# Kernel optimization log

Hardware: AMD Instinct MI355X
Metric: run time of the kernel (lower is better)

## Reference

```python
import jax, jax.numpy as jnp
import numpy as np

B, N = 65536, 8
OBS0, OBS1, OBS2 = 6, 1024, 7
H, HC, NA = 64, 128, 2


def _glorot(key, shape):
    fan_in = shape[0]
    lim = 1.0 / np.sqrt(fan_in)
    return jax.random.uniform(key, shape, jnp.float32, -lim, lim)


def setup_inputs() -> dict:
    key = jax.random.key(0)
    ks = jax.random.split(key, 24)
    state0 = jax.random.normal(ks[0], (B, OBS0), jnp.float32)
    state1 = jax.random.normal(ks[1], (B, OBS1), jnp.float32)
    state2 = jax.random.normal(ks[2], (B, N, OBS2), jnp.float32)
    keep = (jax.random.uniform(ks[3], (B, N, 1)) > 0.35) | (jnp.arange(N)[None, :, None] == 0)
    state2 = state2 * keep.astype(jnp.float32)
    return {
        "state0": state0, "state1": state1, "state2": state2,
        "W0": _glorot(ks[4], (OBS0, H)), "b0": jnp.zeros((H,), jnp.float32),
        "Wg": _glorot(ks[5], (OBS1, H)), "bg": jnp.zeros((H,), jnp.float32),
        "Ws1": _glorot(ks[6], (OBS2, H)), "bs1": jnp.zeros((H,), jnp.float32),
        "Ws2": _glorot(ks[7], (H, H)), "bs2": jnp.zeros((H,), jnp.float32),
        "Wq": _glorot(ks[8], (H, H)),
        "Wk": _glorot(ks[9], (H, H)),
        "Wv": _glorot(ks[10], (H, H)),
        "Wc1": _glorot(ks[11], (3 * H, HC)), "bc1": jnp.zeros((HC,), jnp.float32),
        "Wc2": _glorot(ks[12], (HC, HC)), "bc2": jnp.zeros((HC,), jnp.float32),
        "Wc3": _glorot(ks[13], (HC, NA)), "bc3": jnp.zeros((NA,), jnp.float32),
    }


def reference(state0, state1, state2,
              W0, b0, Wg, bg, Ws1, bs1, Ws2, bs2,
              Wq, Wk, Wv, Wc1, bc1, Wc2, bc2, Wc3, bc3):
    own_e = jax.nn.relu(state0 @ W0 + b0)                      # [B, 64]
    env_e = jax.nn.relu(state1 @ Wg + bg)                      # [B, 64]
    intru_e = jax.nn.relu(state2 @ Ws1 + bs1)                  # [B, N, 64]
    intru_e = jax.nn.relu(intru_e @ Ws2 + bs2)                 # [B, N, 64]

    q = own_e @ Wq                                             # [B, 64]
    k = intru_e @ Wk                                           # [B, N, 64]
    v = intru_e @ Wv                                           # [B, N, 64]

    # mask: True where the neighbor slot is non-padding (mean over feats != 0)
    mask = jnp.mean(state2, axis=2, keepdims=True) != 0        # [B, N, 1] bool

    score = jnp.einsum('bnd,bd->bn', k, q)[..., None]          # [B, N, 1]
    score_m = jnp.where(mask, score, -jnp.inf)
    alpha = jax.nn.softmax(score_m / np.sqrt(H), axis=1)       # [B, N, 1]
    alpha_m = jnp.where(mask, alpha, 0.0)
    v_att = jnp.sum(v * alpha_m, axis=1)                       # [B, 64]

    concat = jnp.concatenate((own_e, env_e, v_att), axis=1)    # [B, 192]
    h = jax.nn.relu(concat @ Wc1 + bc1)
    h = jax.nn.relu(h @ Wc2 + bc2)
    return jnp.tanh(h @ Wc3 + bc3)                             # [B, n_actions]
```

## Files before the change

### kernel.cpp

```cpp
#include <hip/hip_runtime.h>
#include <math.h>


typedef float f32x4 __attribute__((ext_vector_type(4)));
typedef float f32x4u __attribute__((ext_vector_type(4), aligned(4)));
typedef float f32x2u __attribute__((ext_vector_type(2), aligned(4)));
typedef __bf16 bf16x8 __attribute__((ext_vector_type(8)));
typedef unsigned short u16x8 __attribute__((ext_vector_type(8)));

#define DI __device__ __forceinline__

DI unsigned short f2bf_u(float f) {
  unsigned u = __builtin_bit_cast(unsigned, f);
  u += 0x7fffu + ((u >> 16) & 1u);
  return (unsigned short)(u >> 16);
}
DI float bfu2f(unsigned short s) {
  unsigned u = ((unsigned)s) << 16;
  return __builtin_bit_cast(float, u);
}
DI u16x8 cvt8(f32x4 x, f32x4 y) {
  bf16x8 r;
  r[0] = (__bf16)x[0]; r[1] = (__bf16)x[1]; r[2] = (__bf16)x[2]; r[3] = (__bf16)x[3];
  r[4] = (__bf16)y[0]; r[5] = (__bf16)y[1]; r[6] = (__bf16)y[2]; r[7] = (__bf16)y[3];
  return __builtin_bit_cast(u16x8, r);
}
DI f32x4 mfma16(u16x8 a, u16x8 b, f32x4 c) {
  return __builtin_amdgcn_mfma_f32_16x16x32_bf16(
      __builtin_bit_cast(bf16x8, a), __builtin_bit_cast(bf16x8, b), c, 0, 0, 0);
}
DI void gload_lds16(const void* g, void* l) {
  typedef __attribute__((address_space(1))) const unsigned GU;
  typedef __attribute__((address_space(3))) unsigned LU;
  __builtin_amdgcn_global_load_lds((GU*)g, (LU*)l, 16, 0, 0);
}


constexpr size_t WS_WGF = 0;
constexpr size_t WS_WS2 = 131072;
constexpr size_t WS_WV  = 139264;
constexpr size_t WS_MQK = 147456;
constexpr size_t WS_WC1 = 155648;
constexpr size_t WS_WC2 = 204800;

__global__ __launch_bounds__(256) void k_prep(
    const float* __restrict__ Wg, const float* __restrict__ Ws2,
    const float* __restrict__ Wv, const float* __restrict__ Wq,
    const float* __restrict__ Wk, const float* __restrict__ Wc1,
    const float* __restrict__ Wc2,
    unsigned short* __restrict__ wgf, unsigned short* __restrict__ ws2f,
    unsigned short* __restrict__ wvf, unsigned short* __restrict__ mqkf,
    unsigned short* __restrict__ wc1f, unsigned short* __restrict__ wc2f) {
  const int idx = blockIdx.x * 256 + threadIdx.x;
  const float* src = nullptr;
  unsigned short* dst;
  int i, ntm, NC;
  bool is_mqk = false;
  if (idx < 65536)      { src = Wg;  dst = wgf;  i = idx;          ntm = 2; NC = 64;  }
  else if (idx < 69632) { src = Ws2; dst = ws2f; i = idx - 65536;  ntm = 2; NC = 64;  }
  else if (idx < 73728) { src = Wv;  dst = wvf;  i = idx - 69632;  ntm = 2; NC = 64;  }
  else if (idx < 77824) { is_mqk = true; dst = mqkf; i = idx - 73728; ntm = 2; NC = 64; }
  else if (idx < 102400){ src = Wc1; dst = wc1f; i = idx - 77824;  ntm = 3; NC = 128; }
  else                  { src = Wc2; dst = wc2f; i = idx - 102400; ntm = 3; NC = 128; }
  const int j = i & 7, ln = (i >> 3) & 63, t2 = i >> 9;
  const int nt = t2 & ((1 << ntm) - 1), kt = t2 >> ntm;
  const int k = kt * 32 + (ln >> 4) * 8 + j, n = nt * 16 + (ln & 15);
  float val;
  if (is_mqk) {
    const f32x4* qp = (const f32x4*)(Wq + k * 64);
    const f32x4* kp = (const f32x4*)(Wk + n * 64);
    float acc = 0.f;
#pragma unroll
    for (int d4 = 0; d4 < 16; ++d4) {
      const f32x4 a = qp[d4], b = kp[d4];
#pragma unroll
      for (int e = 0; e < 4; ++e) acc = fmaf(a[e], b[e], acc);
    }
    val = acc;
  } else {
    val = src[k * NC + n];
  }
  dst[i] = f2bf_u(val);
}

__global__ __launch_bounds__(256, 3) void k_main(
    const float* __restrict__ s0, const float* __restrict__ s1,
    const float* __restrict__ s2,
    const float* __restrict__ W0, const float* __restrict__ b0v,
    const unsigned short* __restrict__ wgf, const float* __restrict__ bg,
    const float* __restrict__ Ws1, const float* __restrict__ bs1,
    const unsigned short* __restrict__ ws2f, const float* __restrict__ bs2,
    const unsigned short* __restrict__ wvf, const unsigned short* __restrict__ mqkf,
    const unsigned short* __restrict__ wc1f, const float* __restrict__ bc1,
    const unsigned short* __restrict__ wc2f, const float* __restrict__ bc2,
    const float* __restrict__ Wc3, const float* __restrict__ bc3,
    float* __restrict__ out) {
  __shared__ __align__(16) char smem[54272];
  u16x8* EF = (u16x8*)smem;
  unsigned short* EFs = (unsigned short*)smem;
  u16x8* H1F = (u16x8*)smem;
  unsigned short* H1Fs = (unsigned short*)smem;
  float* H2 = (float*)(smem + 8192);
  u16x8* CF = (u16x8*)(smem + 32768);
  unsigned short* CFs = (unsigned short*)(smem + 32768);
  float* QK = (float*)(smem + 45056);
  u16x8* SEF = (u16x8*)(smem + 45056);
  float* SC = (float*)(smem + 53248);

  const int tid = threadIdx.x;
  const int lane = tid & 63, wave = tid >> 6;
  const int lo = lane & 15, q = lane >> 4;
  const int bbase = blockIdx.x * 32;

  const int bl8 = tid >> 3, n8 = tid & 7;
  const float* s2p = s2 + ((size_t)(bbase + bl8) * 8 + n8) * 7;
  const f32x4u x03 = *(const f32x4u*)s2p;
  const f32x2u x45 = *(const f32x2u*)(s2p + 4);
  const float x6 = s2p[6];
  const float* s0p = s0 + (size_t)(bbase + bl8) * 6;
  const f32x4u y03 = *(const f32x4u*)s0p;
  const f32x2u y45 = *(const f32x2u*)(s0p + 4);

  {
    const int mt = wave & 1, ntb = wave >> 1;
    const char* s1b = (const char*)(s1 + (size_t)bbase * 1024);

    int srow[4], scol[4];
#pragma unroll
    for (int i = 0; i < 4; ++i) {
      const int T = (i * 256 + tid) * 16;
      srow[i] = T >> 9;
      scol[i] = (T & 511) ^ ((srow[i] & 7) << 4);
    }
    auto stage = [&](char* dst, int c) {
      const int srcb = c * 512;
#pragma unroll
      for (int i = 0; i < 4; ++i)
        gload_lds16(s1b + (size_t)srow[i] * 4096 + srcb + scol[i],
                    dst + (i * 256 + tid) * 16);
    };

    f32x4 acc0 = {}, acc1 = {};
    const int row = mt * 16 + lo;
    const int sw = (row & 7) << 4;
    const u16x8* wgfp = (const u16x8*)wgf + (ntb * 2) * 64 + lane;

    auto compute = [&](const char* src, int c) {
#pragma unroll
      for (int kt = 0; kt < 4; ++kt) {
        const int base = row * 512 + kt * 128 + q * 32;
        const f32x4 alo = *(const f32x4*)(src + (base ^ sw));
        const f32x4 ahi = *(const f32x4*)(src + ((base + 16) ^ sw));
        const int ktg = c * 4 + kt;
        const u16x8 b0 = wgfp[(ktg * 4 + 0) * 64];
        const u16x8 b1 = wgfp[(ktg * 4 + 1) * 64];
        const u16x8 af = cvt8(alo, ahi);
        acc0 = mfma16(af, b0, acc0);
        acc1 = mfma16(af, b1, acc1);
      }
    };

    stage(smem, 0);
    __syncthreads();
#pragma unroll
    for (int cc = 0; cc < 4; ++cc) {
      stage(smem + 16384, cc * 2 + 1);
      compute(smem, cc * 2);
      __syncthreads();
      if (cc < 3) stage(smem, cc * 2 + 2);
      compute(smem + 16384, cc * 2 + 1);
      __syncthreads();
    }

#pragma unroll
    for (int ni = 0; ni < 2; ++ni) {
      const f32x4 a = ni ? acc1 : acc0;
      const int h = (ntb * 2 + ni) * 16 + lo;
      const float bias = bg[h];
#pragma unroll
      for (int ri = 0; ri < 4; ++ri) {
        const float v = fmaxf(a[ri] + bias, 0.f);
        CFs[((mt * 6 + 2 + (h >> 5)) * 64 +
             ((((h >> 3) & 3) << 4) | (q * 4 + ri))) * 8 + (h & 7)] = f2bf_u(v);
      }
    }
  }

  bool maskreg;
  {
    float xv[7] = {x03[0], x03[1], x03[2], x03[3], x45[0], x45[1], x6};
    const float sum = xv[0] + xv[1] + xv[2] + xv[3] + xv[4] + xv[5] + xv[6];
    maskreg = (sum != 0.f);
    const int mt = tid >> 4, rl = tid & 15;
#pragma unroll
    for (int c = 0; c < 8; ++c) {
      float a[8];
#pragma unroll
      for (int i = 0; i < 8; ++i) a[i] = bs1[c * 8 + i];
#pragma unroll
      for (int j = 0; j < 7; ++j) {
        const float* wr = Ws1 + j * 64 + c * 8;
#pragma unroll
        for (int i = 0; i < 8; ++i) a[i] = fmaf(xv[j], wr[i], a[i]);
      }
      u16x8 pk;
#pragma unroll
      for (int i = 0; i < 8; ++i) pk[i] = f2bf_u(fmaxf(a[i], 0.f));
      EF[(mt * 2 + (c >> 2)) * 64 + (((c & 3) << 4) | rl)] = pk;
    }
  }
  __syncthreads();

  {
    u16x8 Bf[4][2];
#pragma unroll
    for (int nt = 0; nt < 4; ++nt)
#pragma unroll
      for (int kt = 0; kt < 2; ++kt)
        Bf[nt][kt] = ((const u16x8*)ws2f)[(kt * 4 + nt) * 64 + lane];
    float bias[4];
#pragma unroll
    for (int nt = 0; nt < 4; ++nt) bias[nt] = bs2[nt * 16 + lo];
#pragma unroll
    for (int mi = 0; mi < 4; ++mi) {
      const int mt = wave * 4 + mi;
      const u16x8 A0 = EF[(mt * 2 + 0) * 64 + lane];
      const u16x8 A1 = EF[(mt * 2 + 1) * 64 + lane];
      f32x4 acc[4] = {};
#pragma unroll
      for (int nt = 0; nt < 4; ++nt) {
        acc[nt] = mfma16(A0, Bf[nt][0], acc[nt]);
        acc[nt] = mfma16(A1, Bf[nt][1], acc[nt]);
      }
#pragma unroll
      for (int nt = 0; nt < 4; ++nt) {
        const int h = nt * 16 + lo;
#pragma unroll
        for (int ri = 0; ri < 4; ++ri) {
          const float v = fmaxf(acc[nt][ri] + bias[nt], 0.f);
          const int rr = mt * 16 + q * 4 + ri;
          EFs[((mt * 2 + (h >> 5)) * 64 + ((((h >> 3) & 3) << 4) | (rr & 15))) * 8 +
              (h & 7)] = f2bf_u(v);
        }
      }
    }
  }
  __syncthreads();

  {
    const int mt = bl8 >> 4, fl = ((n8 & 3) << 4) | (bl8 & 15), kt = n8 >> 2;
    const float yv[6] = {y03[0], y03[1], y03[2], y03[3], y45[0], y45[1]};
    float a[8];
#pragma unroll
    for (int i = 0; i < 8; ++i) a[i] = b0v[n8 * 8 + i];
#pragma unroll
    for (int j = 0; j < 6; ++j) {
      const float* wr = W0 + j * 64 + n8 * 8;
#pragma unroll
      for (int i = 0; i < 8; ++i) a[i] = fmaf(yv[j], wr[i], a[i]);
    }
    u16x8 pk;
#pragma unroll
    for (int i = 0; i < 8; ++i) pk[i] = f2bf_u(fmaxf(a[i], 0.f));
    CF[(mt * 6 + kt) * 64 + fl] = pk;
  }
  __syncthreads();

  {
#pragma unroll
    for (int pp = 0; pp < 2; ++pp) {
      const int pr = wave * 2 + pp, mt = pr >> 2, nt = pr & 3;
      const u16x8 A0 = CF[(mt * 6 + 0) * 64 + lane];
      const u16x8 A1 = CF[(mt * 6 + 1) * 64 + lane];
      const u16x8 B0 = ((const u16x8*)mqkf)[(0 * 4 + nt) * 64 + lane];
      const u16x8 B1 = ((const u16x8*)mqkf)[(1 * 4 + nt) * 64 + lane];
      f32x4 acc = {};
      acc = mfma16(A0, B0, acc);
      acc = mfma16(A1, B1, acc);
#pragma unroll
      for (int ri = 0; ri < 4; ++ri)
        QK[(mt * 16 + q * 4 + ri) * 64 + nt * 16 + lo] = acc[ri];
    }
  }
  __syncthreads();

  {
    const int r = tid, bl = r >> 3, mt = r >> 4, rl = r & 15;
    float dot = 0.f;
#pragma unroll
    for (int c = 0; c < 8; ++c) {
      const u16x8 e = EF[(mt * 2 + (c >> 2)) * 64 + (((c & 3) << 4) | rl)];
      const float* qkp = QK + bl * 64 + c * 8;
      const f32x4 qa = *(const f32x4*)(qkp);
      const f32x4 qb = *(const f32x4*)(qkp + 4);
#pragma unroll
      for (int i = 0; i < 4; ++i) dot = fmaf(bfu2f(e[i]), qa[i], dot);
#pragma unroll
      for (int i = 0; i < 4; ++i) dot = fmaf(bfu2f(e[4 + i]), qb[i], dot);
    }
    SC[r] = maskreg ? dot * 0.125f : -1e30f;
  }
  __syncthreads();

  if (tid < 32) {
    float s[8];
#pragma unroll
    for (int n = 0; n < 8; ++n) s[n] = SC[tid * 8 + n];
    float mx = s[0];
#pragma unroll
    for (int n = 1; n < 8; ++n) mx = fmaxf(mx, s[n]);
    float e[8], sum = 0.f;
#pragma unroll
    for (int n = 0; n < 8; ++n) { e[n] = __expf(s[n] - mx); sum += e[n]; }
    const float inv = 1.f / sum;
#pragma unroll
    for (int n = 0; n < 8; ++n) SC[tid * 8 + n] = e[n] * inv;
  }
  __syncthreads();

  {
    float al[8];
#pragma unroll
    for (int n = 0; n < 8; ++n) al[n] = SC[bl8 * 8 + n];
    float a[8] = {0.f, 0.f, 0.f, 0.f, 0.f, 0.f, 0.f, 0.f};
#pragma unroll
    for (int n = 0; n < 8; ++n) {
      const int rr = bl8 * 8 + n;
      const u16x8 e =
          EF[((rr >> 4) * 2 + (n8 >> 2)) * 64 + (((n8 & 3) << 4) | (rr & 15))];
#pragma unroll
      for (int i = 0; i < 8; ++i) a[i] = fmaf(al[n], bfu2f(e[i]), a[i]);
    }
    u16x8 pk;
#pragma unroll
    for (int i = 0; i < 8; ++i) pk[i] = f2bf_u(a[i]);
    SEF[((bl8 >> 4) * 2 + (n8 >> 2)) * 64 + (((n8 & 3) << 4) | (bl8 & 15))] = pk;
  }
  __syncthreads();

  {
#pragma unroll
    for (int pp = 0; pp < 2; ++pp) {
      const int pr = wave * 2 + pp, mt = pr >> 2, nt = pr & 3;
      const u16x8 A0 = SEF[(mt * 2 + 0) * 64 + lane];
      const u16x8 A1 = SEF[(mt * 2 + 1) * 64 + lane];
      const u16x8 B0 = ((const u16x8*)wvf)[(0 * 4 + nt) * 64 + lane];
      const u16x8 B1 = ((const u16x8*)wvf)[(1 * 4 + nt) * 64 + lane];
      f32x4 acc = {};
      acc = mfma16(A0, B0, acc);
      acc = mfma16(A1, B1, acc);
      const int h = nt * 16 + lo;
#pragma unroll
      for (int ri = 0; ri < 4; ++ri) {
        const int rr = mt * 16 + q * 4 + ri;
        CFs[((mt * 6 + 4 + (h >> 5)) * 64 + ((((h >> 3) & 3) << 4) | (rr & 15))) * 8 +
            (h & 7)] = f2bf_u(acc[ri]);
      }
    }
  }
  __syncthreads();

  {
    const int mt = wave & 1, ntb = (wave >> 1) * 4;
    u16x8 A[6];
#pragma unroll
    for (int kt = 0; kt < 6; ++kt) A[kt] = CF[(mt * 6 + kt) * 64 + lane];
#pragma unroll
    for (int ni = 0; ni < 4; ++ni) {
      const int nt = ntb + ni;
      f32x4 acc = {};
#pragma unroll
      for (int kt = 0; kt < 6; ++kt) {
        const u16x8 Bf = ((const u16x8*)wc1f)[(kt * 8 + nt) * 64 + lane];
        acc = mfma16(A[kt], Bf, acc);
      }
      const float bias = bc1[nt * 16 + lo];
      const int h = nt * 16 + lo;
#pragma unroll
      for (int ri = 0; ri < 4; ++ri) {
        const float v = fmaxf(acc[ri] + bias, 0.f);
        const int rr = mt * 16 + q * 4 + ri;
        H1Fs[((mt * 4 + (h >> 5)) * 64 + ((((h >> 3) & 3) << 4) | (rr & 15))) * 8 +
             (h & 7)] = f2bf_u(v);
      }
    }
  }
  __syncthreads();

  {
    const int mt = wave & 1, ntb = (wave >> 1) * 4;
    u16x8 A[4];
#pragma unroll
    for (int kt = 0; kt < 4; ++kt) A[kt] = H1F[(mt * 4 + kt) * 64 + lane];
#pragma unroll
    for (int ni = 0; ni < 4; ++ni) {
      const int nt = ntb + ni;
      f32x4 acc = {};
#pragma unroll
      for (int kt = 0; kt < 4; ++kt) {
        const u16x8 Bf = ((const u16x8*)wc2f)[(kt * 8 + nt) * 64 + lane];
        acc = mfma16(A[kt], Bf, acc);
      }
      const float bias = bc2[nt * 16 + lo];
#pragma unroll
      for (int ri = 0; ri < 4; ++ri)
        H2[(mt * 16 + q * 4 + ri) * 132 + nt * 16 + lo] =
            fmaxf(acc[ri] + bias, 0.f);
    }
  }
  __syncthreads();

  {
    const int kq = n8 >> 1, a = n8 & 1;
    const f32x4* h4 = (const f32x4*)(H2 + bl8 * 132 + kq * 32);
    const float* wr = Wc3 + kq * 64;
    float acc = 0.f;
#pragma unroll
    for (int j4 = 0; j4 < 8; ++j4) {
      const f32x4 hv = h4[j4];
#pragma unroll
      for (int e = 0; e < 4; ++e) acc = fmaf(hv[e], wr[(j4 * 4 + e) * 2 + a], acc);
    }
    acc += __shfl_down(acc, 2);
    acc += __shfl_down(acc, 4);
    if (kq == 0) out[(size_t)(bbase + bl8) * 2 + a] = tanhf(acc + bc3[a]);
  }
}

extern "C" void kernel_launch(void* const* d_in, const int* in_sizes, int n_in,
                              void* d_out, int out_size, void* d_ws, size_t ws_size,
                              hipStream_t stream) {
  const float* s0  = (const float*)d_in[0];
  const float* s1  = (const float*)d_in[1];
  const float* s2  = (const float*)d_in[2];
  const float* W0  = (const float*)d_in[3];
  const float* b0  = (const float*)d_in[4];
  const float* Wg  = (const float*)d_in[5];
  const float* bg  = (const float*)d_in[6];
  const float* Ws1 = (const float*)d_in[7];
  const float* bs1 = (const float*)d_in[8];
  const float* Ws2 = (const float*)d_in[9];
  const float* bs2 = (const float*)d_in[10];
  const float* Wq  = (const float*)d_in[11];
  const float* Wk  = (const float*)d_in[12];
  const float* Wv  = (const float*)d_in[13];
  const float* Wc1 = (const float*)d_in[14];
  const float* bc1 = (const float*)d_in[15];
  const float* Wc2 = (const float*)d_in[16];
  const float* bc2 = (const float*)d_in[17];
  const float* Wc3 = (const float*)d_in[18];
  const float* bc3 = (const float*)d_in[19];

  char* ws = (char*)d_ws;
  unsigned short* wgf  = (unsigned short*)(ws + WS_WGF);
  unsigned short* ws2f = (unsigned short*)(ws + WS_WS2);
  unsigned short* wvf  = (unsigned short*)(ws + WS_WV);
  unsigned short* mqkf = (unsigned short*)(ws + WS_MQK);
  unsigned short* wc1f = (unsigned short*)(ws + WS_WC1);
  unsigned short* wc2f = (unsigned short*)(ws + WS_WC2);

  hipLaunchKernelGGL(k_prep, dim3(464), dim3(256), 0, stream, Wg, Ws2, Wv, Wq,
                     Wk, Wc1, Wc2, wgf, ws2f, wvf, mqkf, wc1f, wc2f);
  hipLaunchKernelGGL(k_main, dim3(2048), dim3(256), 0, stream, s0, s1, s2, W0,
                     b0, wgf, bg, Ws1, bs1, ws2f, bs2, wvf, mqkf, wc1f, bc1,
                     wc2f, bc2, Wc3, bc3, (float*)d_out);
}
```

Before: 453.4 us.

## Restructure per-wave staging and wave-local attention to cut block barriers

The state1 GEMM now stages a private 8KB LDS buffer per wave, with k split across wave pairs and reduced through LDS, replacing the block-wide double-buffered pipeline and its many __syncthreads. Each wave now owns a 16-row M tile through the attention stages. own_e stays in registers and feeds both the q projection and the Wc1 GEMM directly. Softmax uses wave shuffles instead of an LDS round trip, which removes several block barriers. The risk is that the per-wave load path waits on vmcnt(0) with no overlap between loading and compute, so memory latency may be exposed.

```diff
diff --git a/kernel.cpp b/kernel.cpp
--- a/kernel.cpp
+++ b/kernel.cpp
@@ -95,7 +95,7 @@
     const unsigned short* __restrict__ wc2f, const float* __restrict__ bc2,
     const float* __restrict__ Wc3, const float* __restrict__ bc3,
     float* __restrict__ out) {
-  __shared__ __align__(16) char smem[54272];
+  __shared__ __align__(16) char smem[53760];
   u16x8* EF = (u16x8*)smem;
   unsigned short* EFs = (unsigned short*)smem;
   u16x8* H1F = (u16x8*)smem;
@@ -103,85 +103,70 @@
   float* H2 = (float*)(smem + 8192);
   u16x8* CF = (u16x8*)(smem + 32768);
   unsigned short* CFs = (unsigned short*)(smem + 32768);
-  float* QK = (float*)(smem + 45056);
-  u16x8* SEF = (u16x8*)(smem + 45056);
-  float* SC = (float*)(smem + 53248);
+  float* QKf = (float*)(smem + 40960);
+  f32x4* RED = (f32x4*)(smem + 40960);
+  u16x8* SEF = (u16x8*)(smem + 49664);
 
   const int tid = threadIdx.x;
   const int lane = tid & 63, wave = tid >> 6;
   const int lo = lane & 15, q = lane >> 4;
   const int bbase = blockIdx.x * 32;
-
   const int bl8 = tid >> 3, n8 = tid & 7;
+  const int mt_q = wave >> 1;
+
   const float* s2p = s2 + ((size_t)(bbase + bl8) * 8 + n8) * 7;
   const f32x4u x03 = *(const f32x4u*)s2p;
   const f32x2u x45 = *(const f32x2u*)(s2p + 4);
   const float x6 = s2p[6];
-  const float* s0p = s0 + (size_t)(bbase + bl8) * 6;
-  const f32x4u y03 = *(const f32x4u*)s0p;
-  const f32x2u y45 = *(const f32x2u*)(s0p + 4);
-
-  {
-    const int mt = wave & 1, ntb = wave >> 1;
-    const char* s1b = (const char*)(s1 + (size_t)bbase * 1024);
-
-    int srow[4], scol[4];
-#pragma unroll
-    for (int i = 0; i < 4; ++i) {
-      const int T = (i * 256 + tid) * 16;
-      srow[i] = T >> 9;
-      scol[i] = (T & 511) ^ ((srow[i] & 7) << 4);
-    }
-    auto stage = [&](char* dst, int c) {
-      const int srcb = c * 512;
-#pragma unroll
-      for (int i = 0; i < 4; ++i)
-        gload_lds16(s1b + (size_t)srow[i] * 4096 + srcb + scol[i],
-                    dst + (i * 256 + tid) * 16);
-    };
-
-    f32x4 acc0 = {}, acc1 = {};
-    const int row = mt * 16 + lo;
-    const int sw = (row & 7) << 4;
-    const u16x8* wgfp = (const u16x8*)wgf + (ntb * 2) * 64 + lane;
-
-    auto compute = [&](const char* src, int c) {
+
+  {
+    const int mt_e = wave & 1, kh = wave >> 1;
+    char* sbuf = smem + wave * 8192;
+    const char* s1b = (const char*)s1 + (size_t)(bbase + mt_e * 16) * 4096 + kh * 2048;
+    const u16x8* wg8 = (const u16x8*)wgf;
+    f32x4 acc[4] = {};
+    const int sw = (lo & 7) << 4;
+    for (int c = 0; c < 4; ++c) {
+      if (c) {
+        asm volatile("s_waitcnt lgkmcnt(0)" ::: "memory");
+      }
+#pragma unroll
+      for (int i = 0; i < 8; ++i) {
+        const int T = (i * 64 + lane) * 16;
+        const int rw = T >> 9, cb = T & 511;
+        gload_lds16(s1b + (size_t)rw * 4096 + c * 512 + (cb ^ ((rw & 7) << 4)),
+                    sbuf + T);
+      }
+      asm volatile("s_waitcnt vmcnt(0)" ::: "memory");
 #pragma unroll
       for (int kt = 0; kt < 4; ++kt) {
-        const int base = row * 512 + kt * 128 + q * 32;
-        const f32x4 alo = *(const f32x4*)(src + (base ^ sw));
-        const f32x4 ahi = *(const f32x4*)(src + ((base + 16) ^ sw));
-        const int ktg = c * 4 + kt;
-        const u16x8 b0 = wgfp[(ktg * 4 + 0) * 64];
-        const u16x8 b1 = wgfp[(ktg * 4 + 1) * 64];
+        const int base = lo * 512 + kt * 128 + q * 32;
+        const f32x4 alo = *(const f32x4*)(sbuf + (base ^ sw));
+        const f32x4 ahi = *(const f32x4*)(sbuf + ((base + 16) ^ sw));
+        const int ktg = kh * 16 + c * 4 + kt;
         const u16x8 af = cvt8(alo, ahi);
-        acc0 = mfma16(af, b0, acc0);
-        acc1 = mfma16(af, b1, acc1);
-      }
-    };
-
-    stage(smem, 0);
+#pragma unroll
+        for (int nt = 0; nt < 4; ++nt)
+          acc[nt] = mfma16(af, wg8[(ktg * 4 + nt) * 64 + lane], acc[nt]);
+      }
+    }
+    if (kh == 1) {
+#pragma unroll
+      for (int nt = 0; nt < 4; ++nt) RED[(mt_e * 4 + nt) * 64 + lane] = acc[nt];
+    }
     __syncthreads();
-#pragma unroll
-    for (int cc = 0; cc < 4; ++cc) {
-      stage(smem + 16384, cc * 2 + 1);
-      compute(smem, cc * 2);
-      __syncthreads();
-      if (cc < 3) stage(smem, cc * 2 + 2);
-      compute(smem + 16384, cc * 2 + 1);
-      __syncthreads();
-    }
-
-#pragma unroll
-    for (int ni = 0; ni < 2; ++ni) {
-      const f32x4 a = ni ? acc1 : acc0;
-      const int h = (ntb * 2 + ni) * 16 + lo;
-      const float bias = bg[h];
-#pragma unroll
-      for (int ri = 0; ri < 4; ++ri) {
-        const float v = fmaxf(a[ri] + bias, 0.f);
-        CFs[((mt * 6 + 2 + (h >> 5)) * 64 +
-             ((((h >> 3) & 3) << 4) | (q * 4 + ri))) * 8 + (h & 7)] = f2bf_u(v);
+    if (kh == 0) {
+#pragma unroll
+      for (int nt = 0; nt < 4; ++nt) {
+        const f32x4 a = acc[nt] + RED[(mt_e * 4 + nt) * 64 + lane];
+        const int h = nt * 16 + lo;
+        const float bias = bg[h];
+#pragma unroll
+        for (int ri = 0; ri < 4; ++ri) {
+          const float v = fmaxf(a[ri] + bias, 0.f);
+          CFs[((mt_e * 4 + (h >> 5)) * 64 +
+               ((((h >> 3) & 3) << 4) | (q * 4 + ri))) * 8 + (h & 7)] = f2bf_u(v);
+        }
       }
     }
   }
@@ -209,15 +194,14 @@
       EF[(mt * 2 + (c >> 2)) * 64 + (((c & 3) << 4) | rl)] = pk;
     }
   }
-  __syncthreads();
-
-  {
+
+  {
+    const u16x8* w2 = (const u16x8*)ws2f;
     u16x8 Bf[4][2];
 #pragma unroll
     for (int nt = 0; nt < 4; ++nt)
 #pragma unroll
-      for (int kt = 0; kt < 2; ++kt)
-        Bf[nt][kt] = ((const u16x8*)ws2f)[(kt * 4 + nt) * 64 + lane];
+      for (int kt = 0; kt < 2; ++kt) Bf[nt][kt] = w2[(kt * 4 + nt) * 64 + lane];
     float bias[4];
 #pragma unroll
     for (int nt = 0; nt < 4; ++nt) bias[nt] = bs2[nt * 16 + lo];
@@ -245,52 +229,53 @@
       }
     }
   }
-  __syncthreads();
-
-  {
-    const int mt = bl8 >> 4, fl = ((n8 & 3) << 4) | (bl8 & 15), kt = n8 >> 2;
-    const float yv[6] = {y03[0], y03[1], y03[2], y03[3], y45[0], y45[1]};
-    float a[8];
-#pragma unroll
-    for (int i = 0; i < 8; ++i) a[i] = b0v[n8 * 8 + i];
-#pragma unroll
-    for (int j = 0; j < 6; ++j) {
-      const float* wr = W0 + j * 64 + n8 * 8;
-#pragma unroll
-      for (int i = 0; i < 8; ++i) a[i] = fmaf(yv[j], wr[i], a[i]);
-    }
-    u16x8 pk;
-#pragma unroll
-    for (int i = 0; i < 8; ++i) pk[i] = f2bf_u(fmaxf(a[i], 0.f));
-    CF[(mt * 6 + kt) * 64 + fl] = pk;
-  }
-  __syncthreads();
-
-  {
-#pragma unroll
-    for (int pp = 0; pp < 2; ++pp) {
-      const int pr = wave * 2 + pp, mt = pr >> 2, nt = pr & 3;
-      const u16x8 A0 = CF[(mt * 6 + 0) * 64 + lane];
-      const u16x8 A1 = CF[(mt * 6 + 1) * 64 + lane];
-      const u16x8 B0 = ((const u16x8*)mqkf)[(0 * 4 + nt) * 64 + lane];
-      const u16x8 B1 = ((const u16x8*)mqkf)[(1 * 4 + nt) * 64 + lane];
+
+  u16x8 cf0, cf1;
+  {
+    const float* s0r = s0 + (size_t)(bbase + mt_q * 16 + lo) * 6;
+    float yv[6];
+#pragma unroll
+    for (int j = 0; j < 6; ++j) yv[j] = s0r[j];
+#pragma unroll
+    for (int half = 0; half < 2; ++half) {
+      const int cb = half * 32 + q * 8;
+      float a[8];
+#pragma unroll
+      for (int i = 0; i < 8; ++i) a[i] = b0v[cb + i];
+#pragma unroll
+      for (int j = 0; j < 6; ++j) {
+        const float* wr = W0 + j * 64 + cb;
+#pragma unroll
+        for (int i = 0; i < 8; ++i) a[i] = fmaf(yv[j], wr[i], a[i]);
+      }
+      u16x8 pk;
+#pragma unroll
+      for (int i = 0; i < 8; ++i) pk[i] = f2bf_u(fmaxf(a[i], 0.f));
+      if (half) cf1 = pk; else cf0 = pk;
+    }
+  }
+
+  {
+    const u16x8* mq8 = (const u16x8*)mqkf;
+#pragma unroll
+    for (int nt = 0; nt < 4; ++nt) {
       f32x4 acc = {};
-      acc = mfma16(A0, B0, acc);
-      acc = mfma16(A1, B1, acc);
+      acc = mfma16(cf0, mq8[(0 * 4 + nt) * 64 + lane], acc);
+      acc = mfma16(cf1, mq8[(1 * 4 + nt) * 64 + lane], acc);
 #pragma unroll
       for (int ri = 0; ri < 4; ++ri)
-        QK[(mt * 16 + q * 4 + ri) * 64 + nt * 16 + lo] = acc[ri];
-    }
-  }
-  __syncthreads();
-
-  {
-    const int r = tid, bl = r >> 3, mt = r >> 4, rl = r & 15;
+        QKf[(mt_q * 16 + q * 4 + ri) * 68 + nt * 16 + lo] = acc[ri];
+    }
+  }
+
+  float score;
+  {
+    const int r = tid, mt = r >> 4, rl = r & 15;
     float dot = 0.f;
 #pragma unroll
     for (int c = 0; c < 8; ++c) {
       const u16x8 e = EF[(mt * 2 + (c >> 2)) * 64 + (((c & 3) << 4) | rl)];
-      const float* qkp = QK + bl * 64 + c * 8;
+      const float* qkp = QKf + bl8 * 68 + c * 8;
       const f32x4 qa = *(const f32x4*)(qkp);
       const f32x4 qb = *(const f32x4*)(qkp + 4);
 #pragma unroll
@@ -298,30 +283,27 @@
 #pragma unroll
       for (int i = 0; i < 4; ++i) dot = fmaf(bfu2f(e[4 + i]), qb[i], dot);
     }
-    SC[r] = maskreg ? dot * 0.125f : -1e30f;
-  }
-  __syncthreads();
-
-  if (tid < 32) {
-    float s[8];
-#pragma unroll
-    for (int n = 0; n < 8; ++n) s[n] = SC[tid * 8 + n];
-    float mx = s[0];
-#pragma unroll
-    for (int n = 1; n < 8; ++n) mx = fmaxf(mx, s[n]);
-    float e[8], sum = 0.f;
-#pragma unroll
-    for (int n = 0; n < 8; ++n) { e[n] = __expf(s[n] - mx); sum += e[n]; }
+    score = maskreg ? dot * 0.125f : -1e30f;
+  }
+
+  float al[8];
+  {
+    const int gb = lane & 56;
+    float sv[8];
+#pragma unroll
+    for (int n = 0; n < 8; ++n) sv[n] = __shfl(score, gb + n, 64);
+    float mx = sv[0];
+#pragma unroll
+    for (int n = 1; n < 8; ++n) mx = fmaxf(mx, sv[n]);
+    float ex[8], sum = 0.f;
+#pragma unroll
+    for (int n = 0; n < 8; ++n) { ex[n] = __expf(sv[n] - mx); sum += ex[n]; }
     const float inv = 1.f / sum;
 #pragma unroll
-    for (int n = 0; n < 8; ++n) SC[tid * 8 + n] = e[n] * inv;
-  }
-  __syncthreads();
-
-  {
-    float al[8];
-#pragma unroll
-    for (int n = 0; n < 8; ++n) al[n] = SC[bl8 * 8 + n];
+    for (int n = 0; n < 8; ++n) al[n] = ex[n] * inv;
+  }
+
+  {
     float a[8] = {0.f, 0.f, 0.f, 0.f, 0.f, 0.f, 0.f, 0.f};
 #pragma unroll
     for (int n = 0; n < 8; ++n) {
@@ -339,48 +321,45 @@
   __syncthreads();
 
   {
-#pragma unroll
-    for (int pp = 0; pp < 2; ++pp) {
-      const int pr = wave * 2 + pp, mt = pr >> 2, nt = pr & 3;
-      const u16x8 A0 = SEF[(mt * 2 + 0) * 64 + lane];
-      const u16x8 A1 = SEF[(mt * 2 + 1) * 64 + lane];
-      const u16x8 B0 = ((const u16x8*)wvf)[(0 * 4 + nt) * 64 + lane];
-      const u16x8 B1 = ((const u16x8*)wvf)[(1 * 4 + nt) * 64 + lane];
+    const u16x8* wv8 = (const u16x8*)wvf;
+    const u16x8 A0 = SEF[(mt_q * 2 + 0) * 64 + lane];
+    const u16x8 A1 = SEF[(mt_q * 2 + 1) * 64 + lane];
+#pragma unroll
+    for (int nt = 0; nt < 4; ++nt) {
       f32x4 acc = {};
-      acc = mfma16(A0, B0, acc);
-      acc = mfma16(A1, B1, acc);
+      acc = mfma16(A0, wv8[(0 * 4 + nt) * 64 + lane], acc);
+      acc = mfma16(A1, wv8[(1 * 4 + nt) * 64 + lane], acc);
       const int h = nt * 16 + lo;
 #pragma unroll
-      for (int ri = 0; ri < 4; ++ri) {
-        const int rr = mt * 16 + q * 4 + ri;
-        CFs[((mt * 6 + 4 + (h >> 5)) * 64 + ((((h >> 3) & 3) << 4) | (rr & 15))) * 8 +
-            (h & 7)] = f2bf_u(acc[ri]);
-      }
-    }
-  }
-  __syncthreads();
-
-  {
-    const int mt = wave & 1, ntb = (wave >> 1) * 4;
-    u16x8 A[6];
-#pragma unroll
-    for (int kt = 0; kt < 6; ++kt) A[kt] = CF[(mt * 6 + kt) * 64 + lane];
+      for (int ri = 0; ri < 4; ++ri)
+        CFs[((mt_q * 4 + 2 + (h >> 5)) * 64 +
+             ((((h >> 3) & 3) << 4) | (q * 4 + ri))) * 8 + (h & 7)] =
+            f2bf_u(acc[ri]);
+    }
+  }
+
+  {
+    const int ntb = (wave & 1) * 4;
+    const u16x8* w18 = (const u16x8*)wc1f;
+    u16x8 A2[4];
+#pragma unroll
+    for (int kt = 0; kt < 4; ++kt) A2[kt] = CF[(mt_q * 4 + kt) * 64 + lane];
 #pragma unroll
     for (int ni = 0; ni < 4; ++ni) {
       const int nt = ntb + ni;
       f32x4 acc = {};
-#pragma unroll
-      for (int kt = 0; kt < 6; ++kt) {
-        const u16x8 Bf = ((const u16x8*)wc1f)[(kt * 8 + nt) * 64 + lane];
-        acc = mfma16(A[kt], Bf, acc);
-      }
+      acc = mfma16(cf0, w18[(0 * 8 + nt) * 64 + lane], acc);
+      acc = mfma16(cf1, w18[(1 * 8 + nt) * 64 + lane], acc);
+#pragma unroll
+      for (int kt = 0; kt < 4; ++kt)
+        acc = mfma16(A2[kt], w18[((2 + kt) * 8 + nt) * 64 + lane], acc);
       const float bias = bc1[nt * 16 + lo];
       const int h = nt * 16 + lo;
 #pragma unroll
       for (int ri = 0; ri < 4; ++ri) {
         const float v = fmaxf(acc[ri] + bias, 0.f);
-        const int rr = mt * 16 + q * 4 + ri;
-        H1Fs[((mt * 4 + (h >> 5)) * 64 + ((((h >> 3) & 3) << 4) | (rr & 15))) * 8 +
+        const int rr = mt_q * 16 + q * 4 + ri;
+        H1Fs[((mt_q * 4 + (h >> 5)) * 64 + ((((h >> 3) & 3) << 4) | (rr & 15))) * 8 +
              (h & 7)] = f2bf_u(v);
       }
     }
@@ -388,23 +367,22 @@
   __syncthreads();
 
   {
-    const int mt = wave & 1, ntb = (wave >> 1) * 4;
+    const int ntb = (wave & 1) * 4;
+    const u16x8* w28 = (const u16x8*)wc2f;
     u16x8 A[4];
 #pragma unroll
-    for (int kt = 0; kt < 4; ++kt) A[kt] = H1F[(mt * 4 + kt) * 64 + lane];
+    for (int kt = 0; kt < 4; ++kt) A[kt] = H1F[(mt_q * 4 + kt) * 64 + lane];
 #pragma unroll
     for (int ni = 0; ni < 4; ++ni) {
       const int nt = ntb + ni;
       f32x4 acc = {};
 #pragma unroll
-      for (int kt = 0; kt < 4; ++kt) {
-        const u16x8 Bf = ((const u16x8*)wc2f)[(kt * 8 + nt) * 64 + lane];
-        acc = mfma16(A[kt], Bf, acc);
-      }
+      for (int kt = 0; kt < 4; ++kt)
+        acc = mfma16(A[kt], w28[(kt * 8 + nt) * 64 + lane], acc);
       const float bias = bc2[nt * 16 + lo];
 #pragma unroll
       for (int ri = 0; ri < 4; ++ri)
-        H2[(mt * 16 + q * 4 + ri) * 132 + nt * 16 + lo] =
+        H2[(mt_q * 16 + q * 4 + ri) * 132 + nt * 16 + lo] =
             fmaxf(acc[ri] + bias, 0.f);
     }
   }
```

Result: no change. 452.5 us (-0.2%).
